# Kernel tuning notes

Measured on AMD Instinct MI355X. Metric: run time of the kernel, lower is better.

Reference implementation:

```python
import jax, jax.numpy as jnp
import numpy as np

N_EMBD = 1024
N_HEAD = 16
HEAD_DIM = N_EMBD // N_HEAD
EPS = 1e-5


def _layer_norm(x, g, b):
    mu = jnp.mean(x, axis=-1, keepdims=True)
    var = jnp.mean(jnp.square(x - mu), axis=-1, keepdims=True)
    return (x - mu) * jax.lax.rsqrt(var + EPS) * g + b


def _gelu_new(x):
    # GPT-2 tanh-approximate GELU
    c = np.sqrt(2.0 / np.pi).astype(np.float32)
    return 0.5 * x * (1.0 + jnp.tanh(c * (x + 0.044715 * x ** 3)))


def setup_inputs() -> dict:
    key = jax.random.key(0)
    ks = jax.random.split(key, 8)
    B, S, D = 8, 1024, N_EMBD
    s = 0.02
    return {
        "x": jax.random.normal(ks[0], (B, S, D), jnp.float32),
        "ln1_g": jnp.ones((D,), jnp.float32),
        "ln1_b": jnp.zeros((D,), jnp.float32),
        "c_attn_w": jax.random.normal(ks[1], (D, 3 * D), jnp.float32) * s,
        "c_attn_b": jnp.zeros((3 * D,), jnp.float32),
        "c_proj_w": jax.random.normal(ks[2], (D, D), jnp.float32) * s,
        "c_proj_b": jnp.zeros((D,), jnp.float32),
        "ln2_g": jnp.ones((D,), jnp.float32),
        "ln2_b": jnp.zeros((D,), jnp.float32),
        "fc_w": jax.random.normal(ks[3], (D, 4 * D), jnp.float32) * s,
        "fc_b": jnp.zeros((4 * D,), jnp.float32),
        "proj_w": jax.random.normal(ks[4], (4 * D, D), jnp.float32) * s,
        "proj_b": jnp.zeros((D,), jnp.float32),
    }


def reference(x, ln1_g, ln1_b, c_attn_w, c_attn_b, c_proj_w, c_proj_b,
              ln2_g, ln2_b, fc_w, fc_b, proj_w, proj_b):
    B, S, D = x.shape
    H, Hd = N_HEAD, HEAD_DIM

    residual = x
    h = _layer_norm(x, ln1_g, ln1_b)

    qkv = h @ c_attn_w + c_attn_b          # [B,S,3D]
    q, k, v = jnp.split(qkv, 3, axis=-1)
    # split heads -> [B,H,S,Hd]
    q = q.reshape(B, S, H, Hd).transpose(0, 2, 1, 3)
    k = k.reshape(B, S, H, Hd).transpose(0, 2, 1, 3)
    v = v.reshape(B, S, H, Hd).transpose(0, 2, 1, 3)

    scores = jnp.einsum('bhqd,bhkd->bhqk', q, k) / jnp.sqrt(
        jnp.asarray(Hd, x.dtype))
    causal = jnp.tril(jnp.ones((S, S), bool))
    mask_value = jnp.finfo(scores.dtype).min
    scores = jnp.where(causal, scores, mask_value)
    attn = jax.nn.softmax(scores, axis=-1)
    ctx = jnp.einsum('bhqk,bhkd->bhqd', attn, v)   # [B,H,S,Hd]
    ctx = ctx.transpose(0, 2, 1, 3).reshape(B, S, D)
    attn_out = ctx @ c_proj_w + c_proj_b

    h = residual + attn_out
    residual = h
    h2 = _layer_norm(h, ln2_g, ln2_b)
    ff = _gelu_new(h2 @ fc_w + fc_b) @ proj_w + proj_b
    return residual + ff
```

## Files before the change

### kernel.cpp

```cpp
#include <hip/hip_runtime.h>
#include <cstdint>
#include <cmath>


#define Bb 8
#define Ss 1024
#define Dd 1024
#define Hh 16
#define HD 64
#define MTOK 8192

typedef __attribute__((ext_vector_type(4))) float  floatx4;
typedef __attribute__((ext_vector_type(8))) short  short8;
typedef __attribute__((ext_vector_type(4))) short  short4v;

__device__ __forceinline__ float bf2f(unsigned short u) {
    return __uint_as_float(((unsigned int)u) << 16);
}
__device__ __forceinline__ unsigned short f2bf(float f) {
    unsigned int u = __float_as_uint(f);
    u += 0x7FFFu + ((u >> 16) & 1u);
    return (unsigned short)(u >> 16);
}

__device__ __forceinline__ void gl2lds16(const void* g, void* l) {
    __builtin_amdgcn_global_load_lds(
        (__attribute__((address_space(1))) void*)(g),
        (__attribute__((address_space(3))) void*)(l),
        16, 0, 0);
}

__global__ __launch_bounds__(256) void pack_w(
    const float* __restrict__ W, unsigned short* __restrict__ P, int K, int N)
{
    const int KC = K >> 5;
    int tile = blockIdx.x * 4 + (threadIdx.x >> 6);
    int lane = threadIdx.x & 63;
    int nt = tile / KC, kc = tile - nt * KC;
    int l16 = lane & 15, quad = lane >> 4;
    const float* src = W + (size_t)(kc * 32 + quad * 8) * N + nt * 16 + l16;
    short8 o;
#pragma unroll
    for (int j = 0; j < 8; ++j) o[j] = (short)f2bf(src[(size_t)j * N]);
    *(short8*)(P + ((size_t)(nt * KC + kc) * 64 + lane) * 8) = o;
}

__global__ __launch_bounds__(256) void layernorm_bf16(
    const float* __restrict__ X, const float* __restrict__ g,
    const float* __restrict__ b, unsigned short* __restrict__ Y)
{
    int row = blockIdx.x, t = threadIdx.x;
    const float4* xr = (const float4*)(X + (size_t)row * Dd);
    float4 v = xr[t];
    float s  = v.x + v.y + v.z + v.w;
    float s2 = v.x * v.x + v.y * v.y + v.z * v.z + v.w * v.w;
#pragma unroll
    for (int off = 32; off >= 1; off >>= 1) {
        s  += __shfl_down(s, off, 64);
        s2 += __shfl_down(s2, off, 64);
    }
    __shared__ float red[8];
    int wave = t >> 6, lane = t & 63;
    if (lane == 0) { red[wave] = s; red[4 + wave] = s2; }
    __syncthreads();
    float ts  = red[0] + red[1] + red[2] + red[3];
    float ts2 = red[4] + red[5] + red[6] + red[7];
    float mu  = ts * (1.0f / Dd);
    float var = ts2 * (1.0f / Dd) - mu * mu;
    float rstd = rsqrtf(var + 1e-5f);
    float4 gv = ((const float4*)g)[t];
    float4 bv = ((const float4*)b)[t];
    ushort4 o;
    o.x = f2bf((v.x - mu) * rstd * gv.x + bv.x);
    o.y = f2bf((v.y - mu) * rstd * gv.y + bv.y);
    o.z = f2bf((v.z - mu) * rstd * gv.z + bv.z);
    o.w = f2bf((v.w - mu) * rstd * gv.w + bv.w);
    ((ushort4*)(Y + (size_t)row * Dd))[t] = o;
}

template <int MODE>
__global__ __launch_bounds__(256, 2) void gemm_fw(
    const unsigned short* __restrict__ A,
    const unsigned short* __restrict__ BP,
    const float* __restrict__ bias,
    const float* __restrict__ res,
    void* __restrict__ out,
    int M, int N, int K)
{
    __shared__ short As[128 * 64];
    const int tid  = threadIdx.x;
    const int wave = tid >> 6, lane = tid & 63;
    const int quad = lane >> 4, l16 = lane & 15;
    const int wm = (wave >> 1) * 64, wn = (wave & 1) * 64;
    const int sw = l16 & 7;
    const size_t rowA0 = (size_t)blockIdx.x * 128;
    const int KC = K >> 5;
    const unsigned short* bb = BP
        + ((size_t)(blockIdx.y * 8 + (wave & 1) * 4) * KC * 512 + (size_t)lane * 8);

    floatx4 acc[4][4] = {};

    int srow[4], scs[4];
#pragma unroll
    for (int r = 0; r < 4; ++r) {
        int idx = tid + r * 256;
        srow[r] = idx >> 3;
        scs[r]  = ((idx & 7) ^ (srow[r] & 7)) * 8;
    }

    for (int k0 = 0; k0 < K; k0 += 64) {
#pragma unroll
        for (int r = 0; r < 4; ++r) {
            int idx = tid + r * 256;
            gl2lds16(A + (rowA0 + srow[r]) * K + k0 + scs[r], As + idx * 8);
        }
        const int kc0 = k0 >> 5;
        short8 bfr[2][4];
#pragma unroll
        for (int ks = 0; ks < 2; ++ks)
#pragma unroll
            for (int ni = 0; ni < 4; ++ni)
                bfr[ks][ni] = *(const short8*)(bb
                    + ((size_t)(ni * KC + kc0 + ks) * 512));
        __syncthreads();

#pragma unroll
        for (int ks = 0; ks < 2; ++ks) {
            short8 af[4];
#pragma unroll
            for (int mi = 0; mi < 4; ++mi)
                af[mi] = *(const short8*)(As + (wm + mi * 16 + l16) * 64
                                             + (((ks << 2) + quad) ^ sw) * 8);
#pragma unroll
            for (int mi = 0; mi < 4; ++mi)
#pragma unroll
                for (int ni = 0; ni < 4; ++ni)
                    acc[mi][ni] = __builtin_amdgcn_mfma_f32_16x16x32_bf16(
                        af[mi], bfr[ks][ni], acc[mi][ni], 0, 0, 0);
        }
        __syncthreads();
    }

#pragma unroll
    for (int mi = 0; mi < 4; ++mi) {
#pragma unroll
        for (int ni = 0; ni < 4; ++ni) {
            size_t row = rowA0 + wm + mi * 16 + quad * 4;
            size_t col = (size_t)blockIdx.y * 128 + wn + ni * 16 + l16;
            float bc = bias[col];
#pragma unroll
            for (int r = 0; r < 4; ++r) {
                float v = acc[mi][ni][r] + bc;
                if (MODE == 0) {
                    ((unsigned short*)out)[(row + r) * N + col] = f2bf(v);
                } else if (MODE == 1) {
                    ((float*)out)[(row + r) * N + col] = v + res[(row + r) * N + col];
                } else {
                    float u = 0.7978845608028654f * (v + 0.044715f * v * v * v);
                    float e = __builtin_amdgcn_exp2f(-2.8853900817779268f * u);
                    float gl = v * __builtin_amdgcn_rcpf(1.0f + e);
                    ((unsigned short*)out)[(row + r) * N + col] = f2bf(gl);
                }
            }
        }
    }
}

__global__ __launch_bounds__(256, 2) void attn_mfma(
    const unsigned short* __restrict__ qkv,
    unsigned short* __restrict__ ctx)
{
    __shared__ unsigned short Ks[64 * 72];
    __shared__ unsigned short VT[64 * 72];
    __shared__ unsigned short PT[128 * 72];

    const int tid  = threadIdx.x;
    const int wave = tid >> 6, lane = tid & 63;
    const int quad = lane >> 4, l16 = lane & 15;
    const int blk = blockIdx.x;
    const int c4 = blk & 3, h = (blk >> 2) & 15, b = blk >> 6;
    const size_t tokbase = (size_t)b * Ss;

    const int skey = tid & 63;
    const int sseg = tid >> 6;

    for (int ci = 0; ci < 2; ++ci) {
        const int chunk = ci ? (7 - c4) : c4;
        const int q0 = chunk * 128;

        short8 qf[2][2];
#pragma unroll
        for (int nb = 0; nb < 2; ++nb)
#pragma unroll
            for (int ks = 0; ks < 2; ++ks) {
                const short8* qp = (const short8*)(qkv
                    + (tokbase + q0 + wave * 32 + nb * 16 + l16) * 3072
                    + h * HD + ks * 32 + quad * 8);
                short8 v = *qp, o;
#pragma unroll
                for (int j = 0; j < 8; ++j)
                    o[j] = (short)f2bf(bf2f((unsigned short)v[j]) * 0.18033688011112042f);
                qf[nb][ks] = o;
            }

        floatx4 Oacc[4][2] = {};
        float mrow[2] = {-3.0e38f, -3.0e38f};
        float lrow[2] = {0.f, 0.f};

        const int nkt = 2 * (chunk + 1);
        for (int kt = 0; kt < nkt; ++kt) {
            __syncthreads();
            {
                const short8* kp = (const short8*)(qkv
                    + (tokbase + kt * 64 + skey) * 3072 + Dd + h * HD + sseg * 16);
                short8 k0 = kp[0], k1 = kp[1];
                *(short8*)(Ks + skey * 72 + sseg * 16)     = k0;
                *(short8*)(Ks + skey * 72 + sseg * 16 + 8) = k1;
                const short8* vp = (const short8*)(qkv
                    + (tokbase + kt * 64 + skey) * 3072 + 2 * Dd + h * HD + sseg * 16);
                short8 v0 = vp[0], v1 = vp[1];
#pragma unroll
                for (int j = 0; j < 8; ++j) {
                    VT[(sseg * 16 + j) * 72 + skey]     = (unsigned short)v0[j];
                    VT[(sseg * 16 + 8 + j) * 72 + skey] = (unsigned short)v1[j];
                }
            }
            __syncthreads();

            floatx4 sacc[4][2] = {};
#pragma unroll
            for (int ks = 0; ks < 2; ++ks) {
                short8 af[4];
#pragma unroll
                for (int mi = 0; mi < 4; ++mi)
                    af[mi] = *(const short8*)(Ks + (mi * 16 + l16) * 72 + ks * 32 + quad * 8);
#pragma unroll
                for (int mi = 0; mi < 4; ++mi)
#pragma unroll
                    for (int nb = 0; nb < 2; ++nb)
                        sacc[mi][nb] = __builtin_amdgcn_mfma_f32_16x16x32_bf16(
                            af[mi], qf[nb][ks], sacc[mi][nb], 0, 0, 0);
            }

            if (kt >= 2 * chunk) {
                const int dk = (kt - 2 * chunk) * 64;
#pragma unroll
                for (int nb = 0; nb < 2; ++nb) {
                    int qrow = wave * 32 + nb * 16 + l16;
#pragma unroll
                    for (int mi = 0; mi < 4; ++mi)
#pragma unroll
                        for (int r = 0; r < 4; ++r)
                            if (dk + mi * 16 + quad * 4 + r > qrow)
                                sacc[mi][nb][r] = -3.0e38f;
                }
            }

#pragma unroll
            for (int nb = 0; nb < 2; ++nb) {
                float mx = sacc[0][nb][0];
#pragma unroll
                for (int mi = 0; mi < 4; ++mi)
#pragma unroll
                    for (int r = 0; r < 4; ++r) mx = fmaxf(mx, sacc[mi][nb][r]);
                mx = fmaxf(mx, __shfl_xor(mx, 16, 64));
                mx = fmaxf(mx, __shfl_xor(mx, 32, 64));
                float mnew  = fmaxf(mrow[nb], mx);
                float alpha = __builtin_amdgcn_exp2f(mrow[nb] - mnew);
                float ls = 0.f;
#pragma unroll
                for (int mi = 0; mi < 4; ++mi) {
                    short4v pk;
#pragma unroll
                    for (int r = 0; r < 4; ++r) {
                        float p = __builtin_amdgcn_exp2f(sacc[mi][nb][r] - mnew);
                        ls += p;
                        pk[r] = (short)f2bf(p);
                    }
                    *(short4v*)(PT + (wave * 32 + nb * 16 + l16) * 72 + mi * 16 + quad * 4) = pk;
                }
                ls += __shfl_xor(ls, 16, 64);
                ls += __shfl_xor(ls, 32, 64);
                lrow[nb] = lrow[nb] * alpha + ls;
                mrow[nb] = mnew;
#pragma unroll
                for (int mi3 = 0; mi3 < 4; ++mi3) Oacc[mi3][nb] *= alpha;
            }
            asm volatile("s_waitcnt lgkmcnt(0)" ::: "memory");

#pragma unroll
            for (int ks2 = 0; ks2 < 2; ++ks2) {
                short8 av[4], bp[2];
#pragma unroll
                for (int mi3 = 0; mi3 < 4; ++mi3)
                    av[mi3] = *(const short8*)(VT + (mi3 * 16 + l16) * 72 + ks2 * 32 + quad * 8);
#pragma unroll
                for (int nb = 0; nb < 2; ++nb)
                    bp[nb] = *(const short8*)(PT + (wave * 32 + nb * 16 + l16) * 72 + ks2 * 32 + quad * 8);
#pragma unroll
                for (int mi3 = 0; mi3 < 4; ++mi3)
#pragma unroll
                    for (int nb = 0; nb < 2; ++nb)
                        Oacc[mi3][nb] = __builtin_amdgcn_mfma_f32_16x16x32_bf16(
                            av[mi3], bp[nb], Oacc[mi3][nb], 0, 0, 0);
            }
        }

#pragma unroll
        for (int nb = 0; nb < 2; ++nb) {
            float inv = 1.0f / lrow[nb];
#pragma unroll
            for (int mi3 = 0; mi3 < 4; ++mi3) {
                short4v ov;
#pragma unroll
                for (int r = 0; r < 4; ++r)
                    ov[r] = (short)f2bf(Oacc[mi3][nb][r] * inv);
                *(short4v*)(PT + (wave * 32 + nb * 16 + l16) * 72 + mi3 * 16 + quad * 4) = ov;
            }
        }
        asm volatile("s_waitcnt lgkmcnt(0)" ::: "memory");
        {
            int ql = lane >> 1, dbase = (lane & 1) * 32;
            unsigned short* op = ctx + (tokbase + q0 + wave * 32 + ql) * Dd + h * HD + dbase;
            const unsigned short* lp = PT + (wave * 32 + ql) * 72 + dbase;
#pragma unroll
            for (int i = 0; i < 4; ++i)
                ((short8*)op)[i] = *(const short8*)(lp + i * 8);
        }
    }
}

extern "C" void kernel_launch(void* const* d_in, const int* in_sizes, int n_in,
                              void* d_out, int out_size, void* d_ws, size_t ws_size,
                              hipStream_t stream)
{
    const float* x        = (const float*)d_in[0];
    const float* ln1_g    = (const float*)d_in[1];
    const float* ln1_b    = (const float*)d_in[2];
    const float* c_attn_w = (const float*)d_in[3];
    const float* c_attn_b = (const float*)d_in[4];
    const float* c_proj_w = (const float*)d_in[5];
    const float* c_proj_b = (const float*)d_in[6];
    const float* ln2_g    = (const float*)d_in[7];
    const float* ln2_b    = (const float*)d_in[8];
    const float* fc_w     = (const float*)d_in[9];
    const float* fc_b     = (const float*)d_in[10];
    const float* proj_w   = (const float*)d_in[11];
    const float* proj_b   = (const float*)d_in[12];
    float* out = (float*)d_out;

    char* p = (char*)d_ws;
    auto alloc = [&](size_t bytes) {
        void* r = (void*)p;
        p += (bytes + 255) & ~(size_t)255;
        return r;
    };
    unsigned short* WaP  = (unsigned short*)alloc((size_t)3072 * 1024 * 2);
    unsigned short* WpP  = (unsigned short*)alloc((size_t)1024 * 1024 * 2);
    unsigned short* WfP  = (unsigned short*)alloc((size_t)4096 * 1024 * 2);
    unsigned short* Wp2P = (unsigned short*)alloc((size_t)1024 * 4096 * 2);
    unsigned short* h1   = (unsigned short*)alloc((size_t)MTOK * 1024 * 2);
    unsigned short* qkv  = (unsigned short*)alloc((size_t)MTOK * 3072 * 2);
    unsigned short* ctx  = (unsigned short*)alloc((size_t)MTOK * 1024 * 2);
    float*          hmid = (float*)alloc((size_t)MTOK * 1024 * 4);
    unsigned short* h2   = (unsigned short*)alloc((size_t)MTOK * 1024 * 2);
    unsigned short* ff1  = (unsigned short*)alloc((size_t)MTOK * 4096 * 2);

    pack_w<<<(3072 / 16) * (1024 / 32) / 4, 256, 0, stream>>>(c_attn_w, WaP, 1024, 3072);
    pack_w<<<(1024 / 16) * (1024 / 32) / 4, 256, 0, stream>>>(c_proj_w, WpP, 1024, 1024);
    pack_w<<<(4096 / 16) * (1024 / 32) / 4, 256, 0, stream>>>(fc_w, WfP, 1024, 4096);
    pack_w<<<(1024 / 16) * (4096 / 32) / 4, 256, 0, stream>>>(proj_w, Wp2P, 4096, 1024);

    layernorm_bf16<<<MTOK, 256, 0, stream>>>(x, ln1_g, ln1_b, h1);
    gemm_fw<0><<<dim3(64, 24), 256, 0, stream>>>(h1, WaP, c_attn_b, nullptr, qkv, MTOK, 3072, 1024);
    attn_mfma<<<Bb * Hh * 4, 256, 0, stream>>>(qkv, ctx);
    gemm_fw<1><<<dim3(64, 8), 256, 0, stream>>>(ctx, WpP, c_proj_b, x, hmid, MTOK, 1024, 1024);
    layernorm_bf16<<<MTOK, 256, 0, stream>>>(hmid, ln2_g, ln2_b, h2);
    gemm_fw<2><<<dim3(64, 32), 256, 0, stream>>>(h2, WfP, fc_b, nullptr, ff1, MTOK, 4096, 1024);
    gemm_fw<1><<<dim3(64, 8), 256, 0, stream>>>(ff1, Wp2P, proj_b, hmid, out, MTOK, 1024, 4096);
}
```

Before: 460.5 us.

## Replace GEMM with triple-buffered LDS pipeline, 512-thread blocks and wider tiles

Rewrites the bf16 GEMM so that both A and packed B tiles are streamed into LDS through a 3-stage ring buffer using direct global-to-LDS loads. Explicit vmcnt waits and raw barriers let the loads for later K steps overlap with the current MFMA work. The kernel moves to 512-thread blocks, with the N tile width (128 or 256) chosen per GEMM and s_setprio raised around the MFMA burst. It targets the load latency exposed by the old single-buffer, barrier-per-step loop, at the cost of more LDS per block and hand-tuned wait counts that must match the number of loads issued.

```diff
diff --git a/kernel.cpp b/kernel.cpp
--- a/kernel.cpp
+++ b/kernel.cpp
@@ -28,6 +28,14 @@
         (__attribute__((address_space(1))) void*)(g),
         (__attribute__((address_space(3))) void*)(l),
         16, 0, 0);
+}
+
+template <int N> __device__ __forceinline__ void wait_vmcnt() {
+    if constexpr (N == 2)       asm volatile("s_waitcnt vmcnt(2)"  ::: "memory");
+    else if constexpr (N == 3)  asm volatile("s_waitcnt vmcnt(3)"  ::: "memory");
+    else if constexpr (N == 6)  asm volatile("s_waitcnt vmcnt(6)"  ::: "memory");
+    else if constexpr (N == 8)  asm volatile("s_waitcnt vmcnt(8)"  ::: "memory");
+    else                        asm volatile("s_waitcnt vmcnt(0)"  ::: "memory");
 }
 
 __global__ __launch_bounds__(256) void pack_w(
@@ -78,8 +86,8 @@
     ((ushort4*)(Y + (size_t)row * Dd))[t] = o;
 }
 
-template <int MODE>
-__global__ __launch_bounds__(256, 2) void gemm_fw(
+template <int MODE, int WC>
+__global__ __launch_bounds__(512, 4) void gemm3b(
     const unsigned short* __restrict__ A,
     const unsigned short* __restrict__ BP,
     const float* __restrict__ bias,
@@ -87,66 +95,87 @@
     void* __restrict__ out,
     int M, int N, int K)
 {
-    __shared__ short As[128 * 64];
+    constexpr int NI  = 4;
+    constexpr int MI  = WC;
+    constexpr int BN  = WC * 64;
+    constexpr int LB  = WC / 2;
+    constexpr int L   = 1 + LB;
+    constexpr int ASZ = 128 * 32;
+    constexpr int BSZ = BN * 32;
+    constexpr int BUF = ASZ + BSZ;
+    __shared__ short LD[3 * BUF];
+
     const int tid  = threadIdx.x;
     const int wave = tid >> 6, lane = tid & 63;
     const int quad = lane >> 4, l16 = lane & 15;
-    const int wm = (wave >> 1) * 64, wn = (wave & 1) * 64;
-    const int sw = l16 & 7;
+    const int wrow = wave / WC, wcol = wave % WC;
     const size_t rowA0 = (size_t)blockIdx.x * 128;
-    const int KC = K >> 5;
-    const unsigned short* bb = BP
-        + ((size_t)(blockIdx.y * 8 + (wave & 1) * 4) * KC * 512 + (size_t)lane * 8);
-
-    floatx4 acc[4][4] = {};
-
-    int srow[4], scs[4];
-#pragma unroll
-    for (int r = 0; r < 4; ++r) {
-        int idx = tid + r * 256;
-        srow[r] = idx >> 3;
-        scs[r]  = ((idx & 7) ^ (srow[r] & 7)) * 8;
-    }
-
-    for (int k0 = 0; k0 < K; k0 += 64) {
-#pragma unroll
-        for (int r = 0; r < 4; ++r) {
-            int idx = tid + r * 256;
-            gl2lds16(A + (rowA0 + srow[r]) * K + k0 + scs[r], As + idx * 8);
-        }
-        const int kc0 = k0 >> 5;
-        short8 bfr[2][4];
-#pragma unroll
-        for (int ks = 0; ks < 2; ++ks)
-#pragma unroll
-            for (int ni = 0; ni < 4; ++ni)
-                bfr[ks][ni] = *(const short8*)(bb
-                    + ((size_t)(ni * KC + kc0 + ks) * 512));
-        __syncthreads();
-
-#pragma unroll
-        for (int ks = 0; ks < 2; ++ks) {
-            short8 af[4];
-#pragma unroll
-            for (int mi = 0; mi < 4; ++mi)
-                af[mi] = *(const short8*)(As + (wm + mi * 16 + l16) * 64
-                                             + (((ks << 2) + quad) ^ sw) * 8);
-#pragma unroll
-            for (int mi = 0; mi < 4; ++mi)
-#pragma unroll
-                for (int ni = 0; ni < 4; ++ni)
-                    acc[mi][ni] = __builtin_amdgcn_mfma_f32_16x16x32_bf16(
-                        af[mi], bfr[ks][ni], acc[mi][ni], 0, 0, 0);
-        }
-        __syncthreads();
-    }
-
-#pragma unroll
-    for (int mi = 0; mi < 4; ++mi) {
-#pragma unroll
-        for (int ni = 0; ni < 4; ++ni) {
-            size_t row = rowA0 + wm + mi * 16 + quad * 4;
-            size_t col = (size_t)blockIdx.y * 128 + wn + ni * 16 + l16;
+    const int NT = K >> 5;
+    const int ntbase = blockIdx.y * (BN >> 4);
+
+    const int rr = tid >> 2, cc = tid & 3;
+    const unsigned short* aSrc = A + (rowA0 + rr) * (size_t)K
+                                   + ((cc ^ ((rr >> 1) & 3)) * 8);
+    const unsigned short* bSrc[LB];
+#pragma unroll
+    for (int r = 0; r < LB; ++r) {
+        int idx = tid + r * 512;
+        bSrc[r] = BP + (size_t)(ntbase + (idx >> 6)) * NT * 512 + (idx & 63) * 8;
+    }
+
+    floatx4 acc[MI][NI] = {};
+
+#pragma unroll
+    for (int g = 0; g < 2; ++g) {
+        gl2lds16(aSrc + g * 32, LD + g * BUF + tid * 8);
+#pragma unroll
+        for (int r = 0; r < LB; ++r)
+            gl2lds16(bSrc[r] + (size_t)g * 512,
+                     LD + g * BUF + ASZ + (tid + r * 512) * 8);
+    }
+    wait_vmcnt<L>();
+    __builtin_amdgcn_s_barrier();
+
+    const int aswz = (l16 >> 1) & 3;
+    int buf = 0;
+    for (int t = 0; t < NT; ++t) {
+        const int ts = (t + 2 < NT) ? t + 2 : NT - 1;
+        int sbuf = buf + 2; if (sbuf >= 3) sbuf -= 3;
+        const short* Ab = LD + buf * BUF;
+        const short* Bt = Ab + ASZ;
+        short8 bfr[NI], af[MI];
+#pragma unroll
+        for (int n = 0; n < NI; ++n)
+            bfr[n] = *(const short8*)(Bt + ((wcol * NI + n) * 64 + lane) * 8);
+#pragma unroll
+        for (int i = 0; i < MI; ++i)
+            af[i] = *(const short8*)(Ab + (wrow * (MI * 16) + i * 16 + l16) * 32
+                                        + ((quad ^ aswz) * 8));
+        gl2lds16(aSrc + (size_t)ts * 32, LD + sbuf * BUF + tid * 8);
+#pragma unroll
+        for (int r = 0; r < LB; ++r)
+            gl2lds16(bSrc[r] + (size_t)ts * 512,
+                     LD + sbuf * BUF + ASZ + (tid + r * 512) * 8);
+        wait_vmcnt<L>();
+        __builtin_amdgcn_s_setprio(1);
+#pragma unroll
+        for (int i = 0; i < MI; ++i)
+#pragma unroll
+            for (int n = 0; n < NI; ++n)
+                acc[i][n] = __builtin_amdgcn_mfma_f32_16x16x32_bf16(
+                    af[i], bfr[n], acc[i][n], 0, 0, 0);
+        __builtin_amdgcn_s_setprio(0);
+        asm volatile("s_barrier" ::: "memory");
+        buf = (buf + 1 == 3) ? 0 : buf + 1;
+    }
+
+    const size_t colB = (size_t)blockIdx.y * BN + wcol * 64;
+#pragma unroll
+    for (int mi = 0; mi < MI; ++mi) {
+#pragma unroll
+        for (int ni = 0; ni < NI; ++ni) {
+            size_t row = rowA0 + wrow * (MI * 16) + mi * 16 + quad * 4;
+            size_t col = colB + ni * 16 + l16;
             float bc = bias[col];
 #pragma unroll
             for (int r = 0; r < 4; ++r) {
@@ -372,10 +401,10 @@
     pack_w<<<(1024 / 16) * (4096 / 32) / 4, 256, 0, stream>>>(proj_w, Wp2P, 4096, 1024);
 
     layernorm_bf16<<<MTOK, 256, 0, stream>>>(x, ln1_g, ln1_b, h1);
-    gemm_fw<0><<<dim3(64, 24), 256, 0, stream>>>(h1, WaP, c_attn_b, nullptr, qkv, MTOK, 3072, 1024);
+    gemm3b<0, 4><<<dim3(64, 12), 512, 0, stream>>>(h1, WaP, c_attn_b, nullptr, qkv, MTOK, 3072, 1024);
     attn_mfma<<<Bb * Hh * 4, 256, 0, stream>>>(qkv, ctx);
-    gemm_fw<1><<<dim3(64, 8), 256, 0, stream>>>(ctx, WpP, c_proj_b, x, hmid, MTOK, 1024, 1024);
+    gemm3b<1, 2><<<dim3(64, 8), 512, 0, stream>>>(ctx, WpP, c_proj_b, x, hmid, MTOK, 1024, 1024);
     layernorm_bf16<<<MTOK, 256, 0, stream>>>(hmid, ln2_g, ln2_b, h2);
-    gemm_fw<2><<<dim3(64, 32), 256, 0, stream>>>(h2, WfP, fc_b, nullptr, ff1, MTOK, 4096, 1024);
-    gemm_fw<1><<<dim3(64, 8), 256, 0, stream>>>(ff1, Wp2P, proj_b, hmid, out, MTOK, 1024, 4096);
-}
+    gemm3b<2, 4><<<dim3(64, 16), 512, 0, stream>>>(h2, WfP, fc_b, nullptr, ff1, MTOK, 4096, 1024);
+    gemm3b<1, 2><<<dim3(64, 8), 512, 0, stream>>>(ff1, Wp2P, proj_b, hmid, out, MTOK, 1024, 4096);
+}
```

After: 442.7 us. 3.9% less time.

## Replace GEMM with triple-buffered LDS pipeline and register-prefetched B fragments

Applied to the files above, without the earlier changes.

Rewrites the bf16 MFMA GEMM to use a 64x256 block tile. A is staged through a 3-slot LDS ring with asynchronous global-to-LDS loads issued two k-steps ahead. B fragments are double-buffered in registers, one 32-wide k-step at a time. Each step uses a single barrier, partial vmcnt waits and s_setprio around the MFMA burst, all aimed at overlapping memory latency with compute. Occupancy is raised to 3 blocks per SM, which risks register pressure and more B reloads per tile.

```diff
diff --git a/kernel.cpp b/kernel.cpp
--- a/kernel.cpp
+++ b/kernel.cpp
@@ -78,8 +78,38 @@
     ((ushort4*)(Y + (size_t)row * Dd))[t] = o;
 }
 
+
+#define RB_ITER(T, CUR, NXT) do {                                             \
+    const int ts_ = ((T) + 2 < NT) ? (T) + 2 : NT - 1;                        \
+    const int tb_ = ((T) + 1 < NT) ? (T) + 1 : NT - 1;                        \
+    const short* Ab_ = As + buf * 2048;                                       \
+    short8 af_[4];                                                            \
+    _Pragma("unroll")                                                         \
+    for (int i_ = 0; i_ < 4; ++i_)                                            \
+        af_[i_] = *(const short8*)(Ab_ + (i_ * 16 + l16) * 32                 \
+                                   + ((quad ^ aswz) * 8));                    \
+    int sbuf_ = buf + 2; if (sbuf_ >= 3) sbuf_ -= 3;                          \
+    gl2lds16(aSrc + (size_t)ts_ * 32, As + sbuf_ * 2048 + tid * 8);           \
+    _Pragma("unroll")                                                         \
+    for (int n_ = 0; n_ < 4; ++n_)                                            \
+        NXT[n_] = *(const short8*)(bSrc + (size_t)n_ * NT * 512               \
+                                   + (size_t)tb_ * 512);                      \
+    asm volatile("s_waitcnt vmcnt(5)" ::: "memory");                          \
+    __builtin_amdgcn_s_setprio(1);                                            \
+    _Pragma("unroll")                                                         \
+    for (int i_ = 0; i_ < 4; ++i_) {                                          \
+        _Pragma("unroll")                                                     \
+        for (int n_ = 0; n_ < 4; ++n_)                                        \
+            acc[i_][n_] = __builtin_amdgcn_mfma_f32_16x16x32_bf16(            \
+                af_[i_], CUR[n_], acc[i_][n_], 0, 0, 0);                      \
+    }                                                                         \
+    __builtin_amdgcn_s_setprio(0);                                            \
+    asm volatile("s_barrier" ::: "memory");                                   \
+    buf = (buf + 1 == 3) ? 0 : buf + 1;                                       \
+} while (0)
+
 template <int MODE>
-__global__ __launch_bounds__(256, 2) void gemm_fw(
+__global__ __launch_bounds__(256, 3) void gemm_rb(
     const unsigned short* __restrict__ A,
     const unsigned short* __restrict__ BP,
     const float* __restrict__ bias,
@@ -87,66 +117,45 @@
     void* __restrict__ out,
     int M, int N, int K)
 {
-    __shared__ short As[128 * 64];
+    __shared__ short As[3 * 2048];
+
     const int tid  = threadIdx.x;
     const int wave = tid >> 6, lane = tid & 63;
     const int quad = lane >> 4, l16 = lane & 15;
-    const int wm = (wave >> 1) * 64, wn = (wave & 1) * 64;
-    const int sw = l16 & 7;
-    const size_t rowA0 = (size_t)blockIdx.x * 128;
-    const int KC = K >> 5;
-    const unsigned short* bb = BP
-        + ((size_t)(blockIdx.y * 8 + (wave & 1) * 4) * KC * 512 + (size_t)lane * 8);
+    const size_t rowA0 = (size_t)blockIdx.x * 64;
+    const int NT = K >> 5;
+
+    const int rr = tid >> 2, cc = tid & 3;
+    const unsigned short* aSrc = A + (rowA0 + rr) * (size_t)K
+                                   + ((cc ^ ((rr >> 1) & 3)) * 8);
+    const unsigned short* bSrc = BP
+        + ((size_t)(blockIdx.y * 16 + wave * 4) * NT) * 512 + (size_t)lane * 8;
 
     floatx4 acc[4][4] = {};
-
-    int srow[4], scs[4];
-#pragma unroll
-    for (int r = 0; r < 4; ++r) {
-        int idx = tid + r * 256;
-        srow[r] = idx >> 3;
-        scs[r]  = ((idx & 7) ^ (srow[r] & 7)) * 8;
+    short8 bfrA[4], bfrB[4];
+
+    gl2lds16(aSrc,      As + tid * 8);
+    gl2lds16(aSrc + 32, As + 2048 + tid * 8);
+#pragma unroll
+    for (int n = 0; n < 4; ++n)
+        bfrA[n] = *(const short8*)(bSrc + (size_t)n * NT * 512);
+    asm volatile("s_waitcnt vmcnt(0)" ::: "memory");
+    __builtin_amdgcn_s_barrier();
+
+    const int aswz = (l16 >> 1) & 3;
+    int buf = 0;
+    for (int t = 0; t < NT; t += 2) {
+        RB_ITER(t,     bfrA, bfrB);
+        RB_ITER(t + 1, bfrB, bfrA);
     }
 
-    for (int k0 = 0; k0 < K; k0 += 64) {
-#pragma unroll
-        for (int r = 0; r < 4; ++r) {
-            int idx = tid + r * 256;
-            gl2lds16(A + (rowA0 + srow[r]) * K + k0 + scs[r], As + idx * 8);
-        }
-        const int kc0 = k0 >> 5;
-        short8 bfr[2][4];
-#pragma unroll
-        for (int ks = 0; ks < 2; ++ks)
-#pragma unroll
-            for (int ni = 0; ni < 4; ++ni)
-                bfr[ks][ni] = *(const short8*)(bb
-                    + ((size_t)(ni * KC + kc0 + ks) * 512));
-        __syncthreads();
-
-#pragma unroll
-        for (int ks = 0; ks < 2; ++ks) {
-            short8 af[4];
-#pragma unroll
-            for (int mi = 0; mi < 4; ++mi)
-                af[mi] = *(const short8*)(As + (wm + mi * 16 + l16) * 64
-                                             + (((ks << 2) + quad) ^ sw) * 8);
-#pragma unroll
-            for (int mi = 0; mi < 4; ++mi)
-#pragma unroll
-                for (int ni = 0; ni < 4; ++ni)
-                    acc[mi][ni] = __builtin_amdgcn_mfma_f32_16x16x32_bf16(
-                        af[mi], bfr[ks][ni], acc[mi][ni], 0, 0, 0);
-        }
-        __syncthreads();
-    }
-
+    const size_t colB = (size_t)blockIdx.y * 256 + wave * 64;
 #pragma unroll
     for (int mi = 0; mi < 4; ++mi) {
 #pragma unroll
         for (int ni = 0; ni < 4; ++ni) {
-            size_t row = rowA0 + wm + mi * 16 + quad * 4;
-            size_t col = (size_t)blockIdx.y * 128 + wn + ni * 16 + l16;
+            size_t row = rowA0 + mi * 16 + quad * 4;
+            size_t col = colB + ni * 16 + l16;
             float bc = bias[col];
 #pragma unroll
             for (int r = 0; r < 4; ++r) {
@@ -372,10 +381,10 @@
     pack_w<<<(1024 / 16) * (4096 / 32) / 4, 256, 0, stream>>>(proj_w, Wp2P, 4096, 1024);
 
     layernorm_bf16<<<MTOK, 256, 0, stream>>>(x, ln1_g, ln1_b, h1);
-    gemm_fw<0><<<dim3(64, 24), 256, 0, stream>>>(h1, WaP, c_attn_b, nullptr, qkv, MTOK, 3072, 1024);
+    gemm_rb<0><<<dim3(128, 12), 256, 0, stream>>>(h1, WaP, c_attn_b, nullptr, qkv, MTOK, 3072, 1024);
     attn_mfma<<<Bb * Hh * 4, 256, 0, stream>>>(qkv, ctx);
-    gemm_fw<1><<<dim3(64, 8), 256, 0, stream>>>(ctx, WpP, c_proj_b, x, hmid, MTOK, 1024, 1024);
+    gemm_rb<1><<<dim3(128, 4), 256, 0, stream>>>(ctx, WpP, c_proj_b, x, hmid, MTOK, 1024, 1024);
     layernorm_bf16<<<MTOK, 256, 0, stream>>>(hmid, ln2_g, ln2_b, h2);
-    gemm_fw<2><<<dim3(64, 32), 256, 0, stream>>>(h2, WfP, fc_b, nullptr, ff1, MTOK, 4096, 1024);
-    gemm_fw<1><<<dim3(64, 8), 256, 0, stream>>>(ff1, Wp2P, proj_b, hmid, out, MTOK, 1024, 4096);
-}
+    gemm_rb<2><<<dim3(128, 16), 256, 0, stream>>>(h2, WfP, fc_b, nullptr, ff1, MTOK, 4096, 1024);
+    gemm_rb<1><<<dim3(128, 4), 256, 0, stream>>>(ff1, Wp2P, proj_b, hmid, out, MTOK, 1024, 4096);
+}
```

Result: no change. 458.7 us (-0.4%).

## Triple-buffer GEMM A and B tiles in LDS with async prefetch

Applied to the files above, without the earlier changes.

Replaces the single-buffered GEMM, which loaded A into LDS and read B straight from global memory into registers, with a three-stage LDS ring buffer. Both A and B tiles are streamed with direct global-to-LDS loads two K-steps ahead, with a single barrier per 32-wide K step. The change also raises occupancy (launch_bounds 3 blocks), adds s_setprio around the MFMA block, and uses a new swizzle for the 32-wide A tile. The goal is to hide global-memory latency behind MFMA work. In exchange it uses 48KB of LDS per block and halves the K step, so barriers are twice as frequent.

```diff
diff --git a/kernel.cpp b/kernel.cpp
--- a/kernel.cpp
+++ b/kernel.cpp
@@ -79,7 +79,7 @@
 }
 
 template <int MODE>
-__global__ __launch_bounds__(256, 2) void gemm_fw(
+__global__ __launch_bounds__(256, 3) void gemm_q4(
     const unsigned short* __restrict__ A,
     const unsigned short* __restrict__ BP,
     const float* __restrict__ bias,
@@ -87,66 +87,82 @@
     void* __restrict__ out,
     int M, int N, int K)
 {
-    __shared__ short As[128 * 64];
+    __shared__ short LD[3 * 8192];
+
     const int tid  = threadIdx.x;
     const int wave = tid >> 6, lane = tid & 63;
     const int quad = lane >> 4, l16 = lane & 15;
-    const int wm = (wave >> 1) * 64, wn = (wave & 1) * 64;
-    const int sw = l16 & 7;
+    const int wrow = wave >> 1, wcol = wave & 1;
     const size_t rowA0 = (size_t)blockIdx.x * 128;
-    const int KC = K >> 5;
-    const unsigned short* bb = BP
-        + ((size_t)(blockIdx.y * 8 + (wave & 1) * 4) * KC * 512 + (size_t)lane * 8);
+    const int NT = K >> 5;
+    const int ntbase = blockIdx.y * 8;
+
+    const unsigned short* aSrc[2];
+    const unsigned short* bSrc[2];
+#pragma unroll
+    for (int r = 0; r < 2; ++r) {
+        int idx = tid + r * 256;
+        int rr = idx >> 2, cc = idx & 3;
+        aSrc[r] = A + (rowA0 + rr) * (size_t)K + ((cc ^ ((rr >> 1) & 3)) * 8);
+        bSrc[r] = BP + (size_t)(ntbase + (idx >> 6)) * NT * 512 + (idx & 63) * 8;
+    }
 
     floatx4 acc[4][4] = {};
 
-    int srow[4], scs[4];
-#pragma unroll
-    for (int r = 0; r < 4; ++r) {
-        int idx = tid + r * 256;
-        srow[r] = idx >> 3;
-        scs[r]  = ((idx & 7) ^ (srow[r] & 7)) * 8;
-    }
-
-    for (int k0 = 0; k0 < K; k0 += 64) {
-#pragma unroll
-        for (int r = 0; r < 4; ++r) {
+#pragma unroll
+    for (int g = 0; g < 2; ++g) {
+#pragma unroll
+        for (int r = 0; r < 2; ++r) {
             int idx = tid + r * 256;
-            gl2lds16(A + (rowA0 + srow[r]) * K + k0 + scs[r], As + idx * 8);
-        }
-        const int kc0 = k0 >> 5;
-        short8 bfr[2][4];
-#pragma unroll
-        for (int ks = 0; ks < 2; ++ks)
-#pragma unroll
-            for (int ni = 0; ni < 4; ++ni)
-                bfr[ks][ni] = *(const short8*)(bb
-                    + ((size_t)(ni * KC + kc0 + ks) * 512));
-        __syncthreads();
-
-#pragma unroll
-        for (int ks = 0; ks < 2; ++ks) {
-            short8 af[4];
-#pragma unroll
-            for (int mi = 0; mi < 4; ++mi)
-                af[mi] = *(const short8*)(As + (wm + mi * 16 + l16) * 64
-                                             + (((ks << 2) + quad) ^ sw) * 8);
-#pragma unroll
-            for (int mi = 0; mi < 4; ++mi)
-#pragma unroll
-                for (int ni = 0; ni < 4; ++ni)
-                    acc[mi][ni] = __builtin_amdgcn_mfma_f32_16x16x32_bf16(
-                        af[mi], bfr[ks][ni], acc[mi][ni], 0, 0, 0);
-        }
-        __syncthreads();
-    }
-
+            gl2lds16(aSrc[r] + g * 32, LD + g * 8192 + idx * 8);
+            gl2lds16(bSrc[r] + (size_t)g * 512, LD + g * 8192 + 4096 + idx * 8);
+        }
+    }
+    asm volatile("s_waitcnt vmcnt(4)" ::: "memory");
+    __builtin_amdgcn_s_barrier();
+
+    const int aswz = (l16 >> 1) & 3;
+    int buf = 0;
+    for (int t = 0; t < NT; ++t) {
+        const int ts = (t + 2 < NT) ? t + 2 : NT - 1;
+        int sbuf = buf + 2; if (sbuf >= 3) sbuf -= 3;
+        const short* Ab = LD + buf * 8192;
+        const short* Bt = Ab + 4096;
+        short8 af[4], bfr[4];
+#pragma unroll
+        for (int i = 0; i < 4; ++i)
+            af[i] = *(const short8*)(Ab + (wrow * 64 + i * 16 + l16) * 32
+                                        + ((quad ^ aswz) * 8));
+#pragma unroll
+        for (int n = 0; n < 4; ++n)
+            bfr[n] = *(const short8*)(Bt + (wcol * 4 + n) * 512 + lane * 8);
+#pragma unroll
+        for (int r = 0; r < 2; ++r) {
+            int idx = tid + r * 256;
+            gl2lds16(aSrc[r] + (size_t)ts * 32, LD + sbuf * 8192 + idx * 8);
+            gl2lds16(bSrc[r] + (size_t)ts * 512,
+                     LD + sbuf * 8192 + 4096 + idx * 8);
+        }
+        asm volatile("s_waitcnt vmcnt(4)" ::: "memory");
+        __builtin_amdgcn_s_setprio(1);
+#pragma unroll
+        for (int i = 0; i < 4; ++i)
+#pragma unroll
+            for (int n = 0; n < 4; ++n)
+                acc[i][n] = __builtin_amdgcn_mfma_f32_16x16x32_bf16(
+                    af[i], bfr[n], acc[i][n], 0, 0, 0);
+        __builtin_amdgcn_s_setprio(0);
+        asm volatile("s_barrier" ::: "memory");
+        buf = (buf + 1 == 3) ? 0 : buf + 1;
+    }
+
+    const size_t colB = (size_t)blockIdx.y * 128 + wcol * 64;
 #pragma unroll
     for (int mi = 0; mi < 4; ++mi) {
 #pragma unroll
         for (int ni = 0; ni < 4; ++ni) {
-            size_t row = rowA0 + wm + mi * 16 + quad * 4;
-            size_t col = (size_t)blockIdx.y * 128 + wn + ni * 16 + l16;
+            size_t row = rowA0 + wrow * 64 + mi * 16 + quad * 4;
+            size_t col = colB + ni * 16 + l16;
             float bc = bias[col];
 #pragma unroll
             for (int r = 0; r < 4; ++r) {
@@ -372,10 +388,10 @@
     pack_w<<<(1024 / 16) * (4096 / 32) / 4, 256, 0, stream>>>(proj_w, Wp2P, 4096, 1024);
 
     layernorm_bf16<<<MTOK, 256, 0, stream>>>(x, ln1_g, ln1_b, h1);
-    gemm_fw<0><<<dim3(64, 24), 256, 0, stream>>>(h1, WaP, c_attn_b, nullptr, qkv, MTOK, 3072, 1024);
+    gemm_q4<0><<<dim3(64, 24), 256, 0, stream>>>(h1, WaP, c_attn_b, nullptr, qkv, MTOK, 3072, 1024);
     attn_mfma<<<Bb * Hh * 4, 256, 0, stream>>>(qkv, ctx);
-    gemm_fw<1><<<dim3(64, 8), 256, 0, stream>>>(ctx, WpP, c_proj_b, x, hmid, MTOK, 1024, 1024);
+    gemm_q4<1><<<dim3(64, 8), 256, 0, stream>>>(ctx, WpP, c_proj_b, x, hmid, MTOK, 1024, 1024);
     layernorm_bf16<<<MTOK, 256, 0, stream>>>(hmid, ln2_g, ln2_b, h2);
-    gemm_fw<2><<<dim3(64, 32), 256, 0, stream>>>(h2, WfP, fc_b, nullptr, ff1, MTOK, 4096, 1024);
-    gemm_fw<1><<<dim3(64, 8), 256, 0, stream>>>(ff1, Wp2P, proj_b, hmid, out, MTOK, 1024, 4096);
-}
+    gemm_q4<2><<<dim3(64, 32), 256, 0, stream>>>(h2, WfP, fc_b, nullptr, ff1, MTOK, 4096, 1024);
+    gemm_q4<1><<<dim3(64, 8), 256, 0, stream>>>(ff1, Wp2P, proj_b, hmid, out, MTOK, 1024, 4096);
+}
```

After: 458.5 us. Within noise of the previous version (-0.4%).
